# Optimization experiments

Measured on AMD Instinct MI355X. Metric: run time of the kernel, lower is better.

## Reference

```python
import jax, jax.numpy as jnp
import numpy as np
from jax import lax

B, S, DM = 4, 4096, 1024
H, P, R = 16, 32, 8
D = DM // H  # head_dim = 64
K_SEL = 4


def setup_inputs() -> dict:
    key = jax.random.key(0)
    ks = jax.random.split(key, 6)
    x = jax.random.normal(ks[0], (B, S, DM), dtype=jnp.float32)
    K_state = jax.random.normal(ks[1], (H, P, R, D), dtype=jnp.float32) / np.sqrt(D)
    V_state = jax.random.normal(ks[2], (H, P, R, D), dtype=jnp.float32) / np.sqrt(D)
    W_router = jax.random.normal(ks[3], (H, D, P), dtype=jnp.float32) / np.sqrt(D)
    W_out = jax.random.normal(ks[4], (DM, DM), dtype=jnp.float32) / np.sqrt(DM)
    b_out = jnp.zeros((DM,), dtype=jnp.float32)
    return {"x": x, "K_state": K_state, "V_state": V_state,
            "W_router": W_router, "W_out": W_out, "b_out": b_out, "k": K_SEL}


def reference(x, K_state, V_state, W_router, W_out, b_out, k):
    b, s, dm = x.shape
    h, p, r, d = K_state.shape
    xh = x.reshape(b, s, h, d)  # per-head token features

    # Router: top-k partition selection per token per head.
    logits = jnp.einsum('bshd,hdp->bshp', xh, W_router)
    topv = lax.top_k(logits, k)[0]            # [b,s,h,k]
    thresh = topv[..., -1:]                   # k-th largest logit
    neg_inf = jnp.array(-jnp.inf, dtype=logits.dtype)
    gates = jax.nn.softmax(jnp.where(logits >= thresh, logits, neg_inf), axis=-1)  # [b,s,h,p], zero off top-k

    # Attention over state rows within each partition (masked-dense == sparse gather math).
    scale = jnp.asarray(1.0 / np.sqrt(d), dtype=x.dtype)
    scores = jnp.einsum('bshd,hprd->bshpr', xh, K_state) * scale
    attn = jax.nn.softmax(scores, axis=-1)    # softmax over rows r within a partition

    # Gate-weighted combine of per-partition attention outputs, fused to avoid [b,s,h,p,d].
    w = attn * gates[..., None]               # [b,s,h,p,r]
    heads = jnp.einsum('bshpr,hprd->bshd', w, V_state)

    out = heads.reshape(b, s, dm) @ W_out + b_out
    return out
```

## Files before the change

kernel.cpp:

```cpp
#include <hip/hip_runtime.h>
#include <hip/hip_bf16.h>

#define BB 4
#define SS 4096
#define DM 1024
#define HH 16
#define PP 32
#define RR 8
#define DD 64
#define NTOK (BB*SS)
#define MM NTOK
#define NN DM
#define KK DM

typedef __attribute__((ext_vector_type(8))) short short8;
typedef __attribute__((ext_vector_type(4))) float floatx4;

static __device__ inline short f2bf(float f) {
    union { __hip_bfloat16 b; short s; } u; u.b = __float2bfloat16(f); return u.s;
}
static __device__ inline short8 pack8(float4 lo, float4 hi) {
    short8 r;
    r[0] = f2bf(lo.x); r[1] = f2bf(lo.y); r[2] = f2bf(lo.z); r[3] = f2bf(lo.w);
    r[4] = f2bf(hi.x); r[5] = f2bf(hi.y); r[6] = f2bf(hi.z); r[7] = f2bf(hi.w);
    return r;
}

static __device__ inline unsigned bfr(float f) {
    unsigned u = __float_as_uint(f);
    return u + 0x7fffu + ((u >> 16) & 1u);
}
static __device__ inline int pk2(float a, float b) {
    return __builtin_amdgcn_perm(bfr(b), bfr(a), 0x07060302);
}
static __device__ inline short8 pk8(float4 lo, float4 hi) {
    union { short8 s; int i[4]; } r;
    r.i[0] = pk2(lo.x, lo.y); r.i[1] = pk2(lo.z, lo.w);
    r.i[2] = pk2(hi.x, hi.y); r.i[3] = pk2(hi.z, hi.w);
    return r.s;
}

__global__ __launch_bounds__(256) void convert_all(const float* __restrict__ Wo,
                                                   const float* __restrict__ Kst,
                                                   const float* __restrict__ Vst,
                                                   __hip_bfloat16* __restrict__ wsw,
                                                   __hip_bfloat16* __restrict__ kfrag,
                                                   __hip_bfloat16* __restrict__ vfrag) {
    if (blockIdx.x < 512) {
        int tid = blockIdx.x * 256 + threadIdx.x;
        int l = tid & 63;
        int kblk = (tid >> 6) & 31;
        int ntile = tid >> 11;
        int col = ntile * 16 + (l & 15);
        int krow = kblk * 32 + (l >> 4) * 8;
#pragma unroll
        for (int j = 0; j < 8; ++j) {
            wsw[(size_t)tid * 8 + j] = __float2bfloat16(Wo[(size_t)(krow + j) * NN + col]);
        }
    } else {
        int tid = (blockIdx.x - 512) * 256 + threadIdx.x;
        int arr = tid >> 15;
        int idx = tid & 32767;
        int h = idx >> 11, blk = (idx >> 6) & 31, fl = idx & 63;
        int fm = fl & 15, fk = fl >> 4;
        short8 val;
        short* dst;
        if (arr == 0) {
            int mt = blk >> 1, kb = blk & 1;
            int pr = mt * 16 + fm, d0 = kb * 32 + fk * 8;
            const float* src = Kst + ((size_t)h * 256 + pr) * 64 + d0;
            float4 lo = *(const float4*)src, hi = *(const float4*)(src + 4);
            val = pack8(lo, hi);
            dst = (short*)kfrag + (size_t)idx * 8;
        } else {
            int mt = blk >> 3, kb = blk & 7;
            int d = mt * 16 + fm, pr0 = kb * 32 + fk * 8;
            const float* src = Vst + ((size_t)h * 256 + pr0) * 64 + d;
#pragma unroll
            for (int j = 0; j < 8; ++j) val[j] = f2bf(src[j * 64]);
            dst = (short*)vfrag + (size_t)idx * 8;
        }
        *(short8*)dst = val;
    }
}

__global__ __launch_bounds__(256) void router_gates(const float* __restrict__ x,
                                                    const float* __restrict__ Wr,
                                                    const int* __restrict__ kp,
                                                    float* __restrict__ gates_g) {
    __shared__ __align__(16) char smem[26624];
    float (*xs)[68] = (float (*)[68])smem;
    float (*Lg)[36] = (float (*)[36])(smem + 17408);

    const int lane = threadIdx.x & 63;
    const int w = threadIdx.x >> 6;
    const int l15 = lane & 15, l4 = lane >> 4;
    const int t0 = blockIdx.x * 64;
    const int h = blockIdx.y;

    {
        int row = threadIdx.x >> 2, q = threadIdx.x & 3;
        const float4* src = (const float4*)(x + (size_t)(t0 + row) * DM + h * 64 + q * 16);
        float4 v0 = src[0], v1 = src[1], v2 = src[2], v3 = src[3];
        float4* dst = (float4*)&xs[row][q * 16];
        dst[0] = v0; dst[1] = v1; dst[2] = v2; dst[3] = v3;
    }

    const int p = lane & 31, dh = lane >> 5;
    float wreg[32];
    {
        const float* wrp = Wr + (size_t)h * (DD * PP) + dh * 32 * PP + p;
#pragma unroll
        for (int dd = 0; dd < 32; ++dd) wreg[dd] = wrp[dd * PP];
    }
    const int kkv = kp[0];

    __syncthreads();

    for (int it = 0; it < 16; it += 2) {
        const int ta = w * 16 + it;
        const int tb = ta + 1;
        float la = 0.f, lb = 0.f;
#pragma unroll
        for (int j = 0; j < 8; ++j) {
            float4 qa = *(const float4*)&xs[ta][dh * 32 + 4 * j];
            float4 qb = *(const float4*)&xs[tb][dh * 32 + 4 * j];
            la += qa.x * wreg[4 * j];     lb += qb.x * wreg[4 * j];
            la += qa.y * wreg[4 * j + 1]; lb += qb.y * wreg[4 * j + 1];
            la += qa.z * wreg[4 * j + 2]; lb += qb.z * wreg[4 * j + 2];
            la += qa.w * wreg[4 * j + 3]; lb += qb.w * wreg[4 * j + 3];
        }
        la += __shfl_xor(la, 32);
        lb += __shfl_xor(lb, 32);
        if (lane < 32) {
            Lg[ta][lane] = la;
            Lg[tb][lane] = lb;
        }
    }
    __syncthreads();

    float thresh = 0.f, a1 = 0.f;
    if (lane < 16) {
        int t = w * 16 + lane;
        float lgr[32];
        const float4* lrow = (const float4*)&Lg[t][0];
#pragma unroll
        for (int c = 0; c < 8; ++c) {
            float4 q4 = lrow[c];
            lgr[4 * c] = q4.x; lgr[4 * c + 1] = q4.y; lgr[4 * c + 2] = q4.z; lgr[4 * c + 3] = q4.w;
        }
        float aa = -INFINITY, b2 = -INFINITY, c3 = -INFINITY, d4 = -INFINITY;
#pragma unroll
        for (int pp = 0; pp < 32; ++pp) {
            float v = lgr[pp];
            float na = fmaxf(aa, v); v = fminf(aa, v); aa = na;
            float nb = fmaxf(b2, v); v = fminf(b2, v); b2 = nb;
            float nc = fmaxf(c3, v); v = fminf(c3, v); c3 = nc;
            d4 = fmaxf(d4, v);
        }
        thresh = (kkv >= 4) ? d4 : (kkv == 3 ? c3 : (kkv == 2 ? b2 : aa));
        a1 = aa;
    }
    thresh = __shfl(thresh, l15);
    a1     = __shfl(a1, l15);

    {
        const int t = w * 16 + l15;
        const int p8 = l4 * 8;
        const float4* lrow = (const float4*)&Lg[t][p8];
        float4 qa = lrow[0], qb = lrow[1];
        float e0 = (qa.x >= thresh) ? __expf(qa.x - a1) : 0.f;
        float e1 = (qa.y >= thresh) ? __expf(qa.y - a1) : 0.f;
        float e2 = (qa.z >= thresh) ? __expf(qa.z - a1) : 0.f;
        float e3 = (qa.w >= thresh) ? __expf(qa.w - a1) : 0.f;
        float e4 = (qb.x >= thresh) ? __expf(qb.x - a1) : 0.f;
        float e5 = (qb.y >= thresh) ? __expf(qb.y - a1) : 0.f;
        float e6 = (qb.z >= thresh) ? __expf(qb.z - a1) : 0.f;
        float e7 = (qb.w >= thresh) ? __expf(qb.w - a1) : 0.f;
        float part = ((e0 + e1) + (e2 + e3)) + ((e4 + e5) + (e6 + e7));
        part += __shfl_xor(part, 16);
        part += __shfl_xor(part, 32);
        float inv = 1.f / part;
        float* gb = gates_g + ((size_t)(h * (NTOK / 64) + blockIdx.x) * 32) * 64 + t;
        gb[(p8 + 0) * 64] = e0 * inv;
        gb[(p8 + 1) * 64] = e1 * inv;
        gb[(p8 + 2) * 64] = e2 * inv;
        gb[(p8 + 3) * 64] = e3 * inv;
        gb[(p8 + 4) * 64] = e4 * inv;
        gb[(p8 + 5) * 64] = e5 * inv;
        gb[(p8 + 6) * 64] = e6 * inv;
        gb[(p8 + 7) * 64] = e7 * inv;
    }
}

__global__ __launch_bounds__(256, 3) void attn_mm(const float* __restrict__ x,
                                                  const __hip_bfloat16* __restrict__ kfrag,
                                                  const __hip_bfloat16* __restrict__ vfrag,
                                                  const float* __restrict__ gates_g,
                                                  __hip_bfloat16* __restrict__ hb) {
    __shared__ __align__(16) short wf[16384];

    const int lane = threadIdx.x & 63;
    const int w = threadIdx.x >> 6;
    const int l15 = lane & 15, l4 = lane >> 4;
    const int t0 = blockIdx.x * 64;
    const int h = blockIdx.y;

    const float* gb = gates_g + ((size_t)(h * (NTOK / 64) + blockIdx.x) * 32) * 64;
    float gv[4][4];
#pragma unroll
    for (int mi = 0; mi < 4; ++mi) {
        const int pidx = (w * 4 + mi) * 2 + (l4 >> 1);
#pragma unroll
        for (int nt = 0; nt < 4; ++nt)
            gv[mi][nt] = gb[pidx * 64 + nt * 16 + l15];
    }

    short8 xb[4][2];
#pragma unroll
    for (int nt = 0; nt < 4; ++nt)
#pragma unroll
        for (int kb = 0; kb < 2; ++kb) {
            const float* bp = x + (size_t)(t0 + nt * 16 + l15) * DM + h * 64 + kb * 32 + l4 * 8;
            float4 lo = *(const float4*)bp;
            float4 hi = *(const float4*)(bp + 4);
            xb[nt][kb] = pk8(lo, hi);
        }
    short8 ka[4][2];
#pragma unroll
    for (int mi = 0; mi < 4; ++mi)
#pragma unroll
        for (int kb = 0; kb < 2; ++kb)
            ka[mi][kb] = *(const short8*)((const short*)kfrag +
                          ((size_t)(h * 32 + (w * 4 + mi) * 2 + kb) * 512 + lane * 8));

    floatx4 acc[4][4] = {};
#pragma unroll
    for (int kb = 0; kb < 2; ++kb)
#pragma unroll
        for (int mi = 0; mi < 4; ++mi)
#pragma unroll
            for (int nt = 0; nt < 4; ++nt)
                acc[mi][nt] = __builtin_amdgcn_mfma_f32_16x16x32_bf16(ka[mi][kb], xb[nt][kb], acc[mi][nt], 0, 0, 0);

#pragma unroll
    for (int mi = 0; mi < 4; ++mi) {
        const int mt = w * 4 + mi;
#pragma unroll
        for (int nt = 0; nt < 4; ++nt) {
            float g = gv[mi][nt];
            float s0 = acc[mi][nt][0] * 0.125f;
            float s1 = acc[mi][nt][1] * 0.125f;
            float s2 = acc[mi][nt][2] * 0.125f;
            float s3 = acc[mi][nt][3] * 0.125f;
            float mx = fmaxf(fmaxf(s0, s1), fmaxf(s2, s3));
            mx = fmaxf(mx, __shfl_xor(mx, 16));
            float e0 = __expf(s0 - mx), e1 = __expf(s1 - mx);
            float e2 = __expf(s2 - mx), e3 = __expf(s3 - mx);
            float loc = (e0 + e1) + (e2 + e3);
            float se = loc + __shfl_xor(loc, 16);
            float ws = g / se;
            int2 pk;
            pk.x = pk2(e0 * ws, e1 * ws);
            pk.y = pk2(e2 * ws, e3 * ws);
            int off = (((mt & 1) * 2 + (l4 >> 1)) * 16 + l15) * 8 + (l4 & 1) * 4;
            *(int2*)&wf[(nt * 8 + (mt >> 1)) * 512 + off] = pk;
        }
    }
    __syncthreads();

    floatx4 h4[4] = {};
#pragma unroll
    for (int kb = 0; kb < 8; ++kb) {
        short8 va = *(const short8*)((const short*)vfrag +
                      ((size_t)(h * 32 + w * 8 + kb) * 512 + lane * 8));
#pragma unroll
        for (int nt = 0; nt < 4; ++nt) {
            short8 wb = *(const short8*)&wf[(nt * 8 + kb) * 512 + lane * 8];
            h4[nt] = __builtin_amdgcn_mfma_f32_16x16x32_bf16(va, wb, h4[nt], 0, 0, 0);
        }
    }
#pragma unroll
    for (int nt = 0; nt < 4; ++nt) {
        int t = t0 + nt * 16 + l15;
        int2 pk;
        pk.x = pk2(h4[nt][0], h4[nt][1]);
        pk.y = pk2(h4[nt][2], h4[nt][3]);
        *(int2*)((short*)hb + (size_t)t * DM + h * 64 + w * 16 + l4 * 4) = pk;
    }
}

__global__ __launch_bounds__(256) void gemm_v5(const __hip_bfloat16* __restrict__ Abf,
                                               const __hip_bfloat16* __restrict__ Bsw,
                                               const float* __restrict__ bias,
                                               float* __restrict__ C) {
    __shared__ __align__(16) short As[2][8192];
    const int lane = threadIdx.x & 63;
    const int wave = threadIdx.x >> 6;
    const int wm = wave >> 1, wn = wave & 1;

    const int wg  = blockIdx.y * 8 + blockIdx.x;
    const int xcd = wg & 7;
    const int loc = wg >> 3;
    const int bm0 = (xcd * 16 + (loc >> 3)) * 128;
    const int bn0 = (loc & 7) * 128;

    const int l15 = lane & 15, l4 = lane >> 4;

    const short* Ap = (const short*)Abf;
    const short* Bp = (const short*)Bsw;

    int crow[4], ck8[4];
#pragma unroll
    for (int j = 0; j < 4; ++j) {
        int c = (wave * 4 + j) * 64 + lane;
        int row = c >> 3;
        crow[j] = row;
        ck8[j] = ((c & 7) ^ (row & 7)) * 8;
    }

    int boff[4];
#pragma unroll
    for (int nt = 0; nt < 4; ++nt)
        boff[nt] = (((bn0 >> 4) + wn * 4 + nt) * 32) * 512 + lane * 8;

    const int axor = l15 & 7;
    int arow[4];
#pragma unroll
    for (int mt = 0; mt < 4; ++mt)
        arow[mt] = (wm * 64 + mt * 16 + l15) * 64;
    const int ak0 = (l4 ^ axor) * 8;
    const int ak1 = ((4 + l4) ^ axor) * 8;

    floatx4 acc[4][4] = {};

#pragma unroll
    for (int j = 0; j < 4; ++j)
        __builtin_amdgcn_global_load_lds(
            (const __attribute__((address_space(1))) unsigned int*)
                (Ap + (size_t)(bm0 + crow[j]) * KK + ck8[j]),
            (__attribute__((address_space(3))) unsigned int*)&As[0][(wave * 4 + j) * 512],
            16, 0, 0);
    short8 bA[4];
#pragma unroll
    for (int nt = 0; nt < 4; ++nt)
        bA[nt] = *(const short8*)(Bp + boff[nt]);
    __syncthreads();

    for (int step = 0; step < 16; ++step) {
        const int cur = step & 1;
        const int nxt = cur ^ 1;

        short8 bB[4];
#pragma unroll
        for (int nt = 0; nt < 4; ++nt)
            bB[nt] = *(const short8*)(Bp + boff[nt] + (size_t)(2 * step + 1) * 512);

        if (step < 15) {
#pragma unroll
            for (int j = 0; j < 4; ++j)
                __builtin_amdgcn_global_load_lds(
                    (const __attribute__((address_space(1))) unsigned int*)
                        (Ap + (size_t)(bm0 + crow[j]) * KK + (step + 1) * 64 + ck8[j]),
                    (__attribute__((address_space(3))) unsigned int*)&As[nxt][(wave * 4 + j) * 512],
                    16, 0, 0);
        }

        short8 a0[4];
#pragma unroll
        for (int mt = 0; mt < 4; ++mt)
            a0[mt] = *(const short8*)&As[cur][arow[mt] + ak0];
#pragma unroll
        for (int mt = 0; mt < 4; ++mt)
#pragma unroll
            for (int nt = 0; nt < 4; ++nt)
                acc[mt][nt] = __builtin_amdgcn_mfma_f32_16x16x32_bf16(a0[mt], bA[nt], acc[mt][nt], 0, 0, 0);

        short8 a1[4];
#pragma unroll
        for (int mt = 0; mt < 4; ++mt)
            a1[mt] = *(const short8*)&As[cur][arow[mt] + ak1];
#pragma unroll
        for (int mt = 0; mt < 4; ++mt)
#pragma unroll
            for (int nt = 0; nt < 4; ++nt)
                acc[mt][nt] = __builtin_amdgcn_mfma_f32_16x16x32_bf16(a1[mt], bB[nt], acc[mt][nt], 0, 0, 0);

        if (step < 15) {
#pragma unroll
            for (int nt = 0; nt < 4; ++nt)
                bA[nt] = *(const short8*)(Bp + boff[nt] + (size_t)(2 * step + 2) * 512);
        }
        __syncthreads();
    }

#pragma unroll
    for (int nt = 0; nt < 4; ++nt) {
        const int col = bn0 + wn * 64 + nt * 16 + l15;
        const float bv = bias[col];
#pragma unroll
        for (int mt = 0; mt < 4; ++mt) {
            const int row0 = bm0 + wm * 64 + mt * 16 + l4 * 4;
#pragma unroll
            for (int i = 0; i < 4; ++i)
                C[(size_t)(row0 + i) * NN + col] = acc[mt][nt][i] + bv;
        }
    }
}

extern "C" void kernel_launch(void* const* d_in, const int* in_sizes, int n_in,
                              void* d_out, int out_size, void* d_ws, size_t ws_size,
                              hipStream_t stream) {
    const float* x   = (const float*)d_in[0];
    const float* Kst = (const float*)d_in[1];
    const float* Vst = (const float*)d_in[2];
    const float* Wr  = (const float*)d_in[3];
    const float* Wo  = (const float*)d_in[4];
    const float* bo  = (const float*)d_in[5];
    const int*   kp  = (const int*)d_in[6];
    float* out = (float*)d_out;

    __hip_bfloat16* hb    = (__hip_bfloat16*)d_ws;
    __hip_bfloat16* wsw   = hb + (size_t)MM * KK;
    __hip_bfloat16* kfrag = wsw + (size_t)KK * NN;
    __hip_bfloat16* vfrag = kfrag + 16 * 32 * 512;
    float* gates_g = (float*)(vfrag + 16 * 32 * 512);

    convert_all<<<dim3(768), 256, 0, stream>>>(Wo, Kst, Vst, wsw, kfrag, vfrag);
    router_gates<<<dim3(NTOK / 64, HH), 256, 0, stream>>>(x, Wr, kp, gates_g);
    attn_mm<<<dim3(NTOK / 64, HH), 256, 0, stream>>>(x, kfrag, vfrag, gates_g, hb);
    gemm_v5<<<dim3(NN / 128, MM / 128), 256, 0, stream>>>(hb, wsw, bo, out);
}
```

Measured before the change: 241.7 us.

## Fuse weight conversion and router into one kernel; pre-convert x to bf16 fragments

Merges convert_all and router_gates into a single pre_fused launch that dispatches on block index. It also adds blocks that convert x into bf16 MFMA fragment layout, stored temporarily in the output buffer. attn_mm then loads prepacked short8 fragments instead of reading fp32 x and packing it. This removes one launch and the conversion work inside attn_mm, at the cost of an extra write and read of the bf16 copy of x and a larger mixed-role grid.

```diff
diff --git a/kernel.cpp b/kernel.cpp
--- a/kernel.cpp
+++ b/kernel.cpp
@@ -40,54 +40,71 @@
     return r.s;
 }
 
-__global__ __launch_bounds__(256) void convert_all(const float* __restrict__ Wo,
-                                                   const float* __restrict__ Kst,
-                                                   const float* __restrict__ Vst,
-                                                   __hip_bfloat16* __restrict__ wsw,
-                                                   __hip_bfloat16* __restrict__ kfrag,
-                                                   __hip_bfloat16* __restrict__ vfrag) {
-    if (blockIdx.x < 512) {
-        int tid = blockIdx.x * 256 + threadIdx.x;
-        int l = tid & 63;
-        int kblk = (tid >> 6) & 31;
-        int ntile = tid >> 11;
-        int col = ntile * 16 + (l & 15);
-        int krow = kblk * 32 + (l >> 4) * 8;
-#pragma unroll
-        for (int j = 0; j < 8; ++j) {
-            wsw[(size_t)tid * 8 + j] = __float2bfloat16(Wo[(size_t)(krow + j) * NN + col]);
-        }
-    } else {
-        int tid = (blockIdx.x - 512) * 256 + threadIdx.x;
-        int arr = tid >> 15;
-        int idx = tid & 32767;
-        int h = idx >> 11, blk = (idx >> 6) & 31, fl = idx & 63;
-        int fm = fl & 15, fk = fl >> 4;
-        short8 val;
-        short* dst;
-        if (arr == 0) {
-            int mt = blk >> 1, kb = blk & 1;
-            int pr = mt * 16 + fm, d0 = kb * 32 + fk * 8;
-            const float* src = Kst + ((size_t)h * 256 + pr) * 64 + d0;
-            float4 lo = *(const float4*)src, hi = *(const float4*)(src + 4);
-            val = pack8(lo, hi);
-            dst = (short*)kfrag + (size_t)idx * 8;
+__global__ __launch_bounds__(256) void pre_fused(const float* __restrict__ x,
+                                                 const float* __restrict__ Wr,
+                                                 const int* __restrict__ kp,
+                                                 const float* __restrict__ Wo,
+                                                 const float* __restrict__ Kst,
+                                                 const float* __restrict__ Vst,
+                                                 float* __restrict__ gates_g,
+                                                 __hip_bfloat16* __restrict__ wsw,
+                                                 __hip_bfloat16* __restrict__ kfrag,
+                                                 __hip_bfloat16* __restrict__ vfrag,
+                                                 __hip_bfloat16* __restrict__ xbf) {
+    const int bx = blockIdx.x;
+
+    if (bx >= 4096) {
+        if (bx < 4608) {
+            int tid = (bx - 4096) * 256 + threadIdx.x;
+            int l = tid & 63;
+            int kblk = (tid >> 6) & 31;
+            int ntile = tid >> 11;
+            int col = ntile * 16 + (l & 15);
+            int krow = kblk * 32 + (l >> 4) * 8;
+#pragma unroll
+            for (int j = 0; j < 8; ++j)
+                wsw[(size_t)tid * 8 + j] = __float2bfloat16(Wo[(size_t)(krow + j) * NN + col]);
+        } else if (bx < 4864) {
+            int tid = (bx - 4608) * 256 + threadIdx.x;
+            int arr = tid >> 15;
+            int idx = tid & 32767;
+            int h = idx >> 11, blk = (idx >> 6) & 31, fl = idx & 63;
+            int fm = fl & 15, fk = fl >> 4;
+            short8 val;
+            short* dst;
+            if (arr == 0) {
+                int mt = blk >> 1, kb = blk & 1;
+                int pr = mt * 16 + fm, d0 = kb * 32 + fk * 8;
+                const float* src = Kst + ((size_t)h * 256 + pr) * 64 + d0;
+                float4 lo = *(const float4*)src, hi = *(const float4*)(src + 4);
+                val = pack8(lo, hi);
+                dst = (short*)kfrag + (size_t)idx * 8;
+            } else {
+                int mt = blk >> 3, kb = blk & 7;
+                int d = mt * 16 + fm, pr0 = kb * 32 + fk * 8;
+                const float* src = Vst + ((size_t)h * 256 + pr0) * 64 + d;
+#pragma unroll
+                for (int j = 0; j < 8; ++j) val[j] = f2bf(src[j * 64]);
+                dst = (short*)vfrag + (size_t)idx * 8;
+            }
+            *(short8*)dst = val;
         } else {
-            int mt = blk >> 3, kb = blk & 7;
-            int d = mt * 16 + fm, pr0 = kb * 32 + fk * 8;
-            const float* src = Vst + ((size_t)h * 256 + pr0) * 64 + d;
-#pragma unroll
-            for (int j = 0; j < 8; ++j) val[j] = f2bf(src[j * 64]);
-            dst = (short*)vfrag + (size_t)idx * 8;
-        }
-        *(short8*)dst = val;
-    }
-}
-
-__global__ __launch_bounds__(256) void router_gates(const float* __restrict__ x,
-                                                    const float* __restrict__ Wr,
-                                                    const int* __restrict__ kp,
-                                                    float* __restrict__ gates_g) {
+            int xid = bx - 4864;
+            int tile = xid & 255, h = xid >> 8;
+            int lane = threadIdx.x & 63, w = threadIdx.x >> 6;
+            int l15 = lane & 15, l4 = lane >> 4;
+            const float* srcb = x + (size_t)(tile * 64 + w * 16 + l15) * DM + h * 64 + l4 * 8;
+            short* dstb = (short*)xbf + ((size_t)((h * 256 + tile) * 8 + w * 2) * 512) + lane * 8;
+#pragma unroll
+            for (int kb = 0; kb < 2; ++kb) {
+                float4 lo = *(const float4*)(srcb + kb * 32);
+                float4 hi = *(const float4*)(srcb + kb * 32 + 4);
+                *(short8*)(dstb + kb * 512) = pk8(lo, hi);
+            }
+        }
+        return;
+    }
+
     __shared__ __align__(16) char smem[26624];
     float (*xs)[68] = (float (*)[68])smem;
     float (*Lg)[36] = (float (*)[36])(smem + 17408);
@@ -95,8 +112,9 @@
     const int lane = threadIdx.x & 63;
     const int w = threadIdx.x >> 6;
     const int l15 = lane & 15, l4 = lane >> 4;
-    const int t0 = blockIdx.x * 64;
-    const int h = blockIdx.y;
+    const int tile = bx & 255;
+    const int h = bx >> 8;
+    const int t0 = tile * 64;
 
     {
         int row = threadIdx.x >> 2, q = threadIdx.x & 3;
@@ -181,7 +199,7 @@
         part += __shfl_xor(part, 16);
         part += __shfl_xor(part, 32);
         float inv = 1.f / part;
-        float* gb = gates_g + ((size_t)(h * (NTOK / 64) + blockIdx.x) * 32) * 64 + t;
+        float* gb = gates_g + ((size_t)(h * 256 + tile) * 32) * 64 + t;
         gb[(p8 + 0) * 64] = e0 * inv;
         gb[(p8 + 1) * 64] = e1 * inv;
         gb[(p8 + 2) * 64] = e2 * inv;
@@ -193,7 +211,7 @@
     }
 }
 
-__global__ __launch_bounds__(256, 3) void attn_mm(const float* __restrict__ x,
+__global__ __launch_bounds__(256, 3) void attn_mm(const __hip_bfloat16* __restrict__ xbf,
                                                   const __hip_bfloat16* __restrict__ kfrag,
                                                   const __hip_bfloat16* __restrict__ vfrag,
                                                   const float* __restrict__ gates_g,
@@ -206,7 +224,7 @@
     const int t0 = blockIdx.x * 64;
     const int h = blockIdx.y;
 
-    const float* gb = gates_g + ((size_t)(h * (NTOK / 64) + blockIdx.x) * 32) * 64;
+    const float* gb = gates_g + ((size_t)(h * 256 + blockIdx.x) * 32) * 64;
     float gv[4][4];
 #pragma unroll
     for (int mi = 0; mi < 4; ++mi) {
@@ -216,16 +234,13 @@
             gv[mi][nt] = gb[pidx * 64 + nt * 16 + l15];
     }
 
+    const short* xbase = (const short*)xbf + ((size_t)(h * 256 + blockIdx.x) * 8) * 512 + lane * 8;
     short8 xb[4][2];
 #pragma unroll
     for (int nt = 0; nt < 4; ++nt)
 #pragma unroll
-        for (int kb = 0; kb < 2; ++kb) {
-            const float* bp = x + (size_t)(t0 + nt * 16 + l15) * DM + h * 64 + kb * 32 + l4 * 8;
-            float4 lo = *(const float4*)bp;
-            float4 hi = *(const float4*)(bp + 4);
-            xb[nt][kb] = pk8(lo, hi);
-        }
+        for (int kb = 0; kb < 2; ++kb)
+            xb[nt][kb] = *(const short8*)(xbase + (nt * 2 + kb) * 512);
     short8 ka[4][2];
 #pragma unroll
     for (int mi = 0; mi < 4; ++mi)
@@ -425,9 +440,10 @@
     __hip_bfloat16* kfrag = wsw + (size_t)KK * NN;
     __hip_bfloat16* vfrag = kfrag + 16 * 32 * 512;
     float* gates_g = (float*)(vfrag + 16 * 32 * 512);
-
-    convert_all<<<dim3(768), 256, 0, stream>>>(Wo, Kst, Vst, wsw, kfrag, vfrag);
-    router_gates<<<dim3(NTOK / 64, HH), 256, 0, stream>>>(x, Wr, kp, gates_g);
-    attn_mm<<<dim3(NTOK / 64, HH), 256, 0, stream>>>(x, kfrag, vfrag, gates_g, hb);
+    __hip_bfloat16* xbf = (__hip_bfloat16*)d_out;
+
+    pre_fused<<<dim3(8960), 256, 0, stream>>>(x, Wr, kp, Wo, Kst, Vst,
+                                              gates_g, wsw, kfrag, vfrag, xbf);
+    attn_mm<<<dim3(NTOK / 64, HH), 256, 0, stream>>>(xbf, kfrag, vfrag, gates_g, hb);
     gemm_v5<<<dim3(NN / 128, MM / 128), 256, 0, stream>>>(hb, wsw, bo, out);
 }
```

After: 227.3 us. -6.0%, faster.
